# Performance work log

Measured on AMD Instinct MI355X. Metric: run time of the kernel, lower is better.

The kernel has to match this reference:

```python
import jax, jax.numpy as jnp
import numpy as np

D_MODEL = 4096
D_FF = 11008


def setup_inputs() -> dict:
    key = jax.random.key(0)
    ks = jax.random.split(key, 7)
    x = jax.random.normal(ks[0], (2, 2048, D_MODEL), dtype=jnp.float32)
    # int8-range quantized weights (stored int32 for portability)
    gate_w = jax.random.randint(ks[1], (D_FF, D_MODEL), -127, 127, dtype=jnp.int32)
    up_w = jax.random.randint(ks[2], (D_FF, D_MODEL), -127, 127, dtype=jnp.int32)
    down_w = jax.random.randint(ks[3], (D_MODEL, D_FF), -127, 127, dtype=jnp.int32)
    # per-output-channel dequant scales (small positive)
    gate_s = jax.random.uniform(ks[4], (D_FF,), dtype=jnp.float32) * 0.01 + 1e-3
    up_s = jax.random.uniform(ks[5], (D_FF,), dtype=jnp.float32) * 0.01 + 1e-3
    down_s = jax.random.uniform(ks[6], (D_MODEL,), dtype=jnp.float32) * 0.01 + 1e-3
    return {"x": x, "gate_w": gate_w, "gate_s": gate_s,
            "up_w": up_w, "up_s": up_s, "down_w": down_w, "down_s": down_s}


def _dequant_linear(x, w_int, scale):
    # y = x @ (scale[:, None] * w).T  ==  (x @ w.T) * scale  (per-row scales)
    return jnp.einsum('bsd,fd->bsf', x, w_int.astype(x.dtype)) * scale


def reference(x, gate_w, gate_s, up_w, up_s, down_w, down_s):
    gate = jax.nn.silu(_dequant_linear(x, gate_w, gate_s))  # [B,S,D_FF]
    up = _dequant_linear(x, up_w, up_s)                     # [B,S,D_FF]
    h = gate * up
    return _dequant_linear(h, down_w, down_s)               # [B,S,D_MODEL]
```

## Files before the change

### kernel.cpp

```cpp
#include <hip/hip_runtime.h>
#include <hip/hip_bf16.h>

#define D_MODEL 4096
#define D_FF    11008
#define NTOK    4096

typedef unsigned int u32;
typedef unsigned short u16;
typedef signed char s8;
using f32x4   = __attribute__((ext_vector_type(4))) float;
using i32x4   = __attribute__((ext_vector_type(4))) int;
using bf16x8  = __attribute__((ext_vector_type(8))) short;
using ushort8 = __attribute__((ext_vector_type(8))) unsigned short;
using u32x2   = __attribute__((ext_vector_type(2))) u32;
using int4v   = __attribute__((ext_vector_type(4))) int;
using float4v = __attribute__((ext_vector_type(4))) float;

__device__ __forceinline__ u16 bf16_rn(float f) {
    u32 u = __builtin_bit_cast(u32, f);
    u += 0x7FFFu + ((u >> 16) & 1u);
    return (u16)(u >> 16);
}
__device__ __forceinline__ u16 bf16_from_int(int v) {
    float f = (float)v;
    return (u16)(__builtin_bit_cast(u32, f) >> 16);
}
__device__ __forceinline__ void gload16(const void* g, void* l) {
    __builtin_amdgcn_global_load_lds(
        (const __attribute__((address_space(1))) u32*)g,
        (__attribute__((address_space(3))) u32*)l, 16, 0, 0);
}

__global__ void k_xscale(const float* __restrict__ x, float* __restrict__ xsc) {
    __shared__ float wmax[4];
    const int row = blockIdx.x;
    const int tid = threadIdx.x;
    const float* p = x + (size_t)row * D_MODEL + tid * 16;
    float m = 0.f;
#pragma unroll
    for (int j = 0; j < 4; ++j) {
        float4v v = *(const float4v*)(p + j * 4);
#pragma unroll
        for (int e = 0; e < 4; ++e) m = fmaxf(m, fabsf(v[e]));
    }
#pragma unroll
    for (int off = 1; off < 64; off <<= 1)
        m = fmaxf(m, __shfl_xor(m, off));
    if ((tid & 63) == 0) wmax[tid >> 6] = m;
    __syncthreads();
    if (tid == 0) {
        m = fmaxf(fmaxf(wmax[0], wmax[1]), fmaxf(wmax[2], wmax[3]));
        xsc[row] = m * (1.0f / 127.0f);
    }
}

__global__ void k_quant_x(const float* __restrict__ x, const float* __restrict__ xsc,
                          s8* __restrict__ xq) {
    int i = (blockIdx.x * 256 + threadIdx.x) * 8;
    const float inv = 1.0f / xsc[i >> 12];
    float4v a = *(const float4v*)(x + i);
    float4v b = *(const float4v*)(x + i + 4);
    u32 w0 = 0, w1 = 0;
#pragma unroll
    for (int e = 0; e < 4; ++e) {
        int qa = (int)rintf(a[e] * inv);
        qa = qa > 127 ? 127 : (qa < -127 ? -127 : qa);
        int qb = (int)rintf(b[e] * inv);
        qb = qb > 127 ? 127 : (qb < -127 ? -127 : qb);
        w0 |= (u32)(qa & 255) << (8 * e);
        w1 |= (u32)(qb & 255) << (8 * e);
    }
    *(u32x2*)(xq + i) = (u32x2){w0, w1};
}

__global__ void k_cvt_w8(const int* __restrict__ w, s8* __restrict__ wb) {
    int i = (blockIdx.x * 256 + threadIdx.x) * 8;
    int4v a = *(const int4v*)(w + i);
    int4v b = *(const int4v*)(w + i + 4);
    u32 w0 = 0, w1 = 0;
#pragma unroll
    for (int e = 0; e < 4; ++e) {
        w0 |= (u32)(a[e] & 255) << (8 * e);
        w1 |= (u32)(b[e] & 255) << (8 * e);
    }
    *(u32x2*)(wb + i) = (u32x2){w0, w1};
}

__global__ void k_cvt_w(const int* __restrict__ w, u16* __restrict__ wb) {
    int i = (blockIdx.x * 256 + threadIdx.x) * 8;
    int4v a = *(const int4v*)(w + i);
    int4v b = *(const int4v*)(w + i + 4);
    ushort8 o;
    o[0] = bf16_from_int(a[0]); o[1] = bf16_from_int(a[1]);
    o[2] = bf16_from_int(a[2]); o[3] = bf16_from_int(a[3]);
    o[4] = bf16_from_int(b[0]); o[5] = bf16_from_int(b[1]);
    o[6] = bf16_from_int(b[2]); o[7] = bf16_from_int(b[3]);
    *(ushort8*)(wb + i) = o;
}


#define BAR   __builtin_amdgcn_s_barrier()
#define PRIO1 __builtin_amdgcn_s_setprio(1)
#define PRIO0 __builtin_amdgcn_s_setprio(0)
#define VMC(N)  asm volatile("s_waitcnt vmcnt(" #N ")" ::: "memory")

#define RD_A8(AA, BUF, MH) {                                                  \
  _Pragma("unroll") for (int mm = 0; mm < 4; ++mm)                            \
    AA[mm] = *(const i32x4*)&lds8[(BUF)*32768 + (MH)*8192 + mm*1024 + adA]; }

#define RD_B8(BB, BUF) {                                                      \
  _Pragma("unroll") for (int nn = 0; nn < 4; ++nn)                            \
    BB[nn] = *(const i32x4*)&lds8[(BUF)*32768 + 16384 + (nn>>1)*8192 +        \
                                  (nn&1)*1024 + adB]; }

#define MFMA_I8(MH, AA, BB)                                                   \
  _Pragma("unroll") for (int mm = 0; mm < 4; ++mm)                            \
  _Pragma("unroll") for (int nn = 0; nn < 4; ++nn)                            \
    acc[(MH)*4+mm][nn] = __builtin_amdgcn_mfma_i32_16x16x64_i8(               \
        AA[mm], BB[nn], acc[(MH)*4+mm][nn], 0, 0, 0);

#define STAGE_AH(BUF, MH, K0) {                                               \
  gload16(xq + (size_t)(bm*256 + (MH)*128 + wave*16 + (lane>>2))*K + (K0) + asw, \
          &lds8[(BUF)*32768 + (MH)*8192 + wave*1024 + lane*16]); }

#define STAGE_B2(BUF, K0) {                                                   \
  gload16(b0base + (size_t)(wave*16 + (lane>>2))*K + (K0) + asw,              \
          &lds8[(BUF)*32768 + 16384 + wave*1024 + lane*16]);                  \
  gload16(b1base + (size_t)(wave*16 + (lane>>2))*K + (K0) + asw,              \
          &lds8[(BUF)*32768 + 24576 + wave*1024 + lane*16]); }

#define TILE_I8(CUR, NXT, T) {                                                \
  RD_A8(a0, CUR, 0); RD_B8(bb, CUR);                                          \
  if ((T)+1 < nt) STAGE_AH(NXT, 1, ((T)+1) << 6);                             \
  BAR; PRIO1; MFMA_I8(0, a0, bb); PRIO0; BAR;                                 \
  RD_A8(a1, CUR, 1);                                                          \
  if ((T)+2 < nt) { STAGE_AH(CUR, 0, ((T)+2) << 6);                           \
                    STAGE_B2(CUR, ((T)+2) << 6); }                            \
  BAR; PRIO1; MFMA_I8(1, a1, bb); PRIO0;                                      \
  if ((T)+2 < nt) { VMC(3); } else { VMC(0); }                                \
  BAR; }

__global__ __launch_bounds__(512, 2) void k_fusedgu_i8(
    const s8* __restrict__ xq,
    const s8* __restrict__ wg8, const s8* __restrict__ wu8,
    const float* __restrict__ gs, const float* __restrict__ us,
    const float* __restrict__ xsc,
    u16* __restrict__ hb, int K, int NBN, int ldc)
{
    __shared__ __align__(16) char lds8[65536];

    const int tid  = threadIdx.x;
    const int lane = tid & 63;
    const int wave = tid >> 6;
    const int wm   = wave >> 2;
    const int wn   = wave & 3;

    const int nwg  = 16 * NBN;
    const int orig = blockIdx.x;
    const int qq   = nwg >> 3, rr = nwg & 7;
    const int xcd  = orig & 7;
    const int swz  = (xcd < rr ? xcd*(qq+1) : rr*(qq+1) + (xcd-rr)*qq) + (orig >> 3);
    const int bm   = swz / NBN;
    const int bn   = swz % NBN;

    const int r    = lane & 15;
    const int sQ   = lane >> 4;
    const int qsw  = (sQ ^ ((r >> 1) & 3)) * 16;
    const int adA  = (wm*64 + r) * 64 + qsw;
    const int adB  = (wn*32 + r) * 64 + qsw;

    const int asw  = ((lane & 3) ^ ((lane >> 3) & 3)) * 16;

    const s8* b0base = wg8 + (size_t)(bn*128) * K;
    const s8* b1base = wu8 + (size_t)(bn*128) * K;

    i32x4 acc[8][4];
#pragma unroll
    for (int m = 0; m < 8; ++m)
#pragma unroll
        for (int n = 0; n < 4; ++n) acc[m][n] = (i32x4){0, 0, 0, 0};

    const int nt = K >> 6;

    STAGE_AH(0, 0, 0); STAGE_AH(0, 1, 0); STAGE_B2(0, 0);
    STAGE_AH(1, 0, 64); STAGE_B2(1, 64);
    VMC(3);
    BAR;

    i32x4 a0[4], a1[4], bb[4];
    for (int t = 0; t < nt; t += 2) {
        TILE_I8(0, 1, t);
        TILE_I8(1, 0, t + 1);
    }

    const int f0 = bn*128 + wn*32 + r;
    const float gsc0 = gs[f0],      usc0 = us[f0];
    const float gsc1 = gs[f0 + 16], usc1 = us[f0 + 16];
#pragma unroll
    for (int m = 0; m < 8; ++m) {
        const int row = bm*256 + (m>>2)*128 + wm*64 + (m&3)*16 + sQ*4;
#pragma unroll
        for (int q = 0; q < 4; ++q) {
            const float xs = xsc[row + q];
            const float g0 = (float)acc[m][0][q] * xs * gsc0;
            const float u0 = (float)acc[m][2][q] * xs * usc0;
            const float g1 = (float)acc[m][1][q] * xs * gsc1;
            const float u1 = (float)acc[m][3][q] * xs * usc1;
            const float h0 = (g0 / (1.0f + __expf(-g0))) * u0;
            const float h1 = (g1 / (1.0f + __expf(-g1))) * u1;
            hb[(size_t)(row + q) * ldc + f0]      = bf16_rn(h0);
            hb[(size_t)(row + q) * ldc + f0 + 16] = bf16_rn(h1);
        }
    }
}


#define READA(AA, BUF, MH) {                                                  \
  _Pragma("unroll") for (int mm = 0; mm < 4; ++mm) {                          \
    AA[mm][0] = *(const bf16x8*)&lds[(BUF)*32768 + (MH)*8192 + mm*1024 + aoffE + g0E]; \
    AA[mm][1] = *(const bf16x8*)&lds[(BUF)*32768 + (MH)*8192 + mm*1024 + aoffE + g1E]; } }

#define READB(BB, BUF, NH) {                                                  \
  _Pragma("unroll") for (int nn = 0; nn < 2; ++nn) {                          \
    BB[nn][0] = *(const bf16x8*)&lds[(BUF)*32768 + 16384 + (NH)*8192 + nn*1024 + boffE + g0E]; \
    BB[nn][1] = *(const bf16x8*)&lds[(BUF)*32768 + 16384 + (NH)*8192 + nn*1024 + boffE + g1E]; } }

#define MFMA16(MH, NH, AA, BB)                                                \
  _Pragma("unroll") for (int mm = 0; mm < 4; ++mm)                            \
  _Pragma("unroll") for (int nn = 0; nn < 2; ++nn)                            \
  _Pragma("unroll") for (int kk = 0; kk < 2; ++kk)                            \
    acc[(MH)*4+mm][(NH)*2+nn] = __builtin_amdgcn_mfma_f32_16x16x32_bf16(      \
        AA[mm][kk], BB[nn][kk], acc[(MH)*4+mm][(NH)*2+nn], 0, 0, 0);

#define REGA(BUF, H) ((BUF)*32768 + (H)*8192)
#define REGB(BUF, H) ((BUF)*32768 + 16384 + (H)*8192)

#define STAGE_A(BUF, MH, K0) {                                                \
  const u16* _s = A + a_sbase + (size_t)(MH)*128*K + (K0);                    \
  gload16(_s,                &lds[REGA(BUF, MH) + wave*512]);                 \
  gload16(_s + (size_t)64*K, &lds[REGA(BUF, MH) + (8+wave)*512]); }

#define STAGE_B(BUF, NH, K0) {                                                \
  const u16* _s = ((NH) ? b1base : b0base) + (K0);                            \
  gload16(_s,                &lds[REGB(BUF, NH) + wave*512]);                 \
  gload16(_s + (size_t)64*K, &lds[REGB(BUF, NH) + (8+wave)*512]); }

#define TILE2(CUR, NXT, T) {                                                  \
  READA(a0, CUR, 0); READB(b0, CUR, 0); READB(b1, CUR, 1);                    \
  if ((T)+1 < nt) STAGE_A(NXT, 1, ((T)+1) << 6);                              \
  BAR; PRIO1;                                                                 \
  MFMA16(0, 0, a0, b0); MFMA16(0, 1, a0, b1);                                 \
  PRIO0; BAR;                                                                 \
  READA(a1, CUR, 1);                                                          \
  if ((T)+2 < nt) { STAGE_A(CUR, 0, ((T)+2) << 6);                            \
                    STAGE_B(CUR, 0, ((T)+2) << 6);                            \
                    STAGE_B(CUR, 1, ((T)+2) << 6); }                          \
  BAR; PRIO1;                                                                 \
  MFMA16(1, 1, a1, b1); MFMA16(1, 0, a1, b0);                                 \
  PRIO0;                                                                      \
  if ((T)+2 < nt) { VMC(6); } else { VMC(0); }                                \
  BAR; }

__global__ __launch_bounds__(512, 2) void k_down256(
    const u16* __restrict__ A, const u16* __restrict__ B0,
    const float* __restrict__ sc0, float* __restrict__ of32,
    int K, int NBN, int ldc)
{
    __shared__ __align__(16) u16 lds[65536];

    const int tid  = threadIdx.x;
    const int lane = tid & 63;
    const int wave = tid >> 6;
    const int wm   = wave >> 2;
    const int wn   = wave & 3;

    const int nwg  = 16 * NBN;
    const int orig = blockIdx.x;
    const int qq   = nwg >> 3, rr = nwg & 7;
    const int xcd  = orig & 7;
    const int swz  = (xcd < rr ? xcd*(qq+1) : rr*(qq+1) + (xcd-rr)*qq) + (orig >> 3);
    const int bm   = swz / NBN;
    const int bn   = swz % NBN;

    const int r    = lane & 15;
    const int sQ   = lane >> 4;
    const int x7   = r & 7;
    const int g0E  = (sQ ^ x7) * 8;
    const int g1E  = ((4 | sQ) ^ x7) * 8;
    const int aoffE = (wm*64 + r) * 64;
    const int boffE = (wn*32 + r) * 64;

    const int lrow = lane >> 3;
    const int goff = ((lane & 7) ^ lrow) * 8;
    const size_t a_sbase = (size_t)(bm*256 + wave*8 + lrow) * K + goff;
    const u16* b0base = B0 + (size_t)(bn*256 +       wave*8 + lrow) * K + goff;
    const u16* b1base = B0 + (size_t)(bn*256 + 128 + wave*8 + lrow) * K + goff;

    f32x4 acc[8][4];
#pragma unroll
    for (int m = 0; m < 8; ++m)
#pragma unroll
        for (int n = 0; n < 4; ++n) acc[m][n] = (f32x4){0.f, 0.f, 0.f, 0.f};

    const int nt = K >> 6;

    STAGE_A(0, 0, 0); STAGE_A(0, 1, 0); STAGE_B(0, 0, 0); STAGE_B(0, 1, 0);
    STAGE_A(1, 0, 64); STAGE_B(1, 0, 64); STAGE_B(1, 1, 64);
    VMC(6);
    BAR;

    bf16x8 a0[4][2], a1[4][2], b0[2][2], b1[2][2];
    for (int t = 0; t < nt; t += 2) {
        TILE2(0, 1, t);
        TILE2(1, 0, t + 1);
    }

#pragma unroll
    for (int n = 0; n < 4; ++n) {
        const int col = bn*256 + (n>>1)*128 + wn*32 + (n&1)*16 + r;
        const float sc = sc0[col];
#pragma unroll
        for (int m = 0; m < 8; ++m) {
            const int row = bm*256 + (m>>2)*128 + wm*64 + (m&3)*16 + sQ*4;
#pragma unroll
            for (int q = 0; q < 4; ++q)
                of32[(size_t)(row + q) * ldc + col] = acc[m][n][q] * sc;
        }
    }
}

extern "C" void kernel_launch(void* const* d_in, const int* in_sizes, int n_in,
                              void* d_out, int out_size, void* d_ws, size_t ws_size,
                              hipStream_t stream) {
    const float* x  = (const float*)d_in[0];
    const int*   gw = (const int*)d_in[1];
    const float* gs = (const float*)d_in[2];
    const int*   uw = (const int*)d_in[3];
    const float* us = (const float*)d_in[4];
    const int*   dw = (const int*)d_in[5];
    const float* ds = (const float*)d_in[6];
    float* out = (float*)d_out;

    const size_t XQ = (size_t)NTOK * D_MODEL;
    const size_t W8 = (size_t)D_FF * D_MODEL;
    const size_t WD = (size_t)D_FF * D_MODEL * 2;
    const size_t HB = (size_t)NTOK * D_FF * 2;
    const size_t SC = (size_t)NTOK * 4;
    if (ws_size < XQ + 2 * W8 + WD + HB + SC) return;

    char* ws = (char*)d_ws;
    s8*  xq   = (s8*)ws;
    s8*  wg8  = (s8*)(ws + XQ);
    s8*  wu8  = (s8*)(ws + XQ + W8);
    u16* wbD  = (u16*)(ws + XQ + 2 * W8);
    u16* hb   = (u16*)(ws + XQ + 2 * W8 + WD);
    float* xsc = (float*)(ws + XQ + 2 * W8 + WD + HB);

    const int wn_elems = D_FF * D_MODEL;
    const int wgrid = wn_elems / (8 * 256);

    k_xscale<<<NTOK, 256, 0, stream>>>(x, xsc);
    k_quant_x<<<(NTOK * D_MODEL) / (8 * 256), 256, 0, stream>>>(x, xsc, xq);
    k_cvt_w8<<<wgrid, 256, 0, stream>>>(gw, wg8);
    k_cvt_w8<<<wgrid, 256, 0, stream>>>(uw, wu8);

    k_fusedgu_i8<<<16 * (D_FF / 128), 512, 0, stream>>>(
        xq, wg8, wu8, gs, us, xsc, hb, D_MODEL, D_FF / 128, D_FF);

    k_cvt_w<<<wgrid, 256, 0, stream>>>(dw, wbD);
    k_down256<<<16 * (D_MODEL / 256), 512, 0, stream>>>(
        hb, wbD, ds, out, D_FF, D_MODEL / 256, D_MODEL);
}
```

Baseline: 851.4 us.

## Fuse x quantization kernels, merge weight converts, overlap down-weight conversion with GEMM

```diff
diff --git a/kernel.cpp b/kernel.cpp
--- a/kernel.cpp
+++ b/kernel.cpp
@@ -4,6 +4,7 @@
 #define D_MODEL 4096
 #define D_FF    11008
 #define NTOK    4096
+#define CVT_BLOCKS 2048
 
 typedef unsigned int u32;
 typedef unsigned short u16;
@@ -31,71 +32,61 @@
         (__attribute__((address_space(3))) u32*)l, 16, 0, 0);
 }
 
-__global__ void k_xscale(const float* __restrict__ x, float* __restrict__ xsc) {
+__global__ void k_prep_x(const float* __restrict__ x, s8* __restrict__ xq,
+                         float* __restrict__ xsc) {
     __shared__ float wmax[4];
     const int row = blockIdx.x;
     const int tid = threadIdx.x;
     const float* p = x + (size_t)row * D_MODEL + tid * 16;
+    float4v v0 = *(const float4v*)(p);
+    float4v v1 = *(const float4v*)(p + 4);
+    float4v v2 = *(const float4v*)(p + 8);
+    float4v v3 = *(const float4v*)(p + 12);
     float m = 0.f;
 #pragma unroll
-    for (int j = 0; j < 4; ++j) {
-        float4v v = *(const float4v*)(p + j * 4);
-#pragma unroll
-        for (int e = 0; e < 4; ++e) m = fmaxf(m, fabsf(v[e]));
-    }
+    for (int e = 0; e < 4; ++e)
+        m = fmaxf(m, fmaxf(fmaxf(fabsf(v0[e]), fabsf(v1[e])),
+                           fmaxf(fabsf(v2[e]), fabsf(v3[e]))));
 #pragma unroll
     for (int off = 1; off < 64; off <<= 1)
         m = fmaxf(m, __shfl_xor(m, off));
     if ((tid & 63) == 0) wmax[tid >> 6] = m;
     __syncthreads();
-    if (tid == 0) {
-        m = fmaxf(fmaxf(wmax[0], wmax[1]), fmaxf(wmax[2], wmax[3]));
-        xsc[row] = m * (1.0f / 127.0f);
-    }
-}
-
-__global__ void k_quant_x(const float* __restrict__ x, const float* __restrict__ xsc,
-                          s8* __restrict__ xq) {
-    int i = (blockIdx.x * 256 + threadIdx.x) * 8;
-    const float inv = 1.0f / xsc[i >> 12];
-    float4v a = *(const float4v*)(x + i);
-    float4v b = *(const float4v*)(x + i + 4);
-    u32 w0 = 0, w1 = 0;
-#pragma unroll
-    for (int e = 0; e < 4; ++e) {
-        int qa = (int)rintf(a[e] * inv);
-        qa = qa > 127 ? 127 : (qa < -127 ? -127 : qa);
-        int qb = (int)rintf(b[e] * inv);
-        qb = qb > 127 ? 127 : (qb < -127 ? -127 : qb);
-        w0 |= (u32)(qa & 255) << (8 * e);
-        w1 |= (u32)(qb & 255) << (8 * e);
-    }
-    *(u32x2*)(xq + i) = (u32x2){w0, w1};
-}
-
-__global__ void k_cvt_w8(const int* __restrict__ w, s8* __restrict__ wb) {
-    int i = (blockIdx.x * 256 + threadIdx.x) * 8;
+    m = fmaxf(fmaxf(wmax[0], wmax[1]), fmaxf(wmax[2], wmax[3]));
+    if (tid == 0) xsc[row] = m * (1.0f / 127.0f);
+    const float inv = (m > 0.f) ? (127.0f / m) : 0.f;
+    i32x4 o;
+    float4v vs[4] = {v0, v1, v2, v3};
+#pragma unroll
+    for (int j = 0; j < 4; ++j) {
+        u32 w = 0;
+#pragma unroll
+        for (int e = 0; e < 4; ++e) {
+            int q = (int)rintf(vs[j][e] * inv);
+            q = q > 127 ? 127 : (q < -127 ? -127 : q);
+            w |= (u32)(q & 255) << (8 * e);
+        }
+        o[j] = (int)w;
+    }
+    *(i32x4*)(xq + (size_t)row * D_MODEL + tid * 16) = o;
+}
+
+__global__ void k_cvt_w8x2(const int* __restrict__ wA, const int* __restrict__ wB,
+                           s8* __restrict__ oA, s8* __restrict__ oB, int halfgrid) {
+    const int b = blockIdx.x;
+    const int* w; s8* o; int bb;
+    if (b < halfgrid) { w = wA; o = oA; bb = b; }
+    else              { w = wB; o = oB; bb = b - halfgrid; }
+    int i = (bb * 256 + threadIdx.x) * 8;
     int4v a = *(const int4v*)(w + i);
-    int4v b = *(const int4v*)(w + i + 4);
+    int4v c = *(const int4v*)(w + i + 4);
     u32 w0 = 0, w1 = 0;
 #pragma unroll
     for (int e = 0; e < 4; ++e) {
         w0 |= (u32)(a[e] & 255) << (8 * e);
-        w1 |= (u32)(b[e] & 255) << (8 * e);
-    }
-    *(u32x2*)(wb + i) = (u32x2){w0, w1};
-}
-
-__global__ void k_cvt_w(const int* __restrict__ w, u16* __restrict__ wb) {
-    int i = (blockIdx.x * 256 + threadIdx.x) * 8;
-    int4v a = *(const int4v*)(w + i);
-    int4v b = *(const int4v*)(w + i + 4);
-    ushort8 o;
-    o[0] = bf16_from_int(a[0]); o[1] = bf16_from_int(a[1]);
-    o[2] = bf16_from_int(a[2]); o[3] = bf16_from_int(a[3]);
-    o[4] = bf16_from_int(b[0]); o[5] = bf16_from_int(b[1]);
-    o[6] = bf16_from_int(b[2]); o[7] = bf16_from_int(b[3]);
-    *(ushort8*)(wb + i) = o;
+        w1 |= (u32)(c[e] & 255) << (8 * e);
+    }
+    *(u32x2*)(o + i) = (u32x2){w0, w1};
 }
 
 
@@ -145,9 +136,27 @@
     const s8* __restrict__ wg8, const s8* __restrict__ wu8,
     const float* __restrict__ gs, const float* __restrict__ us,
     const float* __restrict__ xsc,
-    u16* __restrict__ hb, int K, int NBN, int ldc)
+    u16* __restrict__ hb, int K, int NBN, int ldc,
+    const int* __restrict__ dw, u16* __restrict__ wbD, int nwgemm)
 {
     __shared__ __align__(16) char lds8[65536];
+
+    if ((int)blockIdx.x >= nwgemm) {
+        const long long tidg = (long long)(blockIdx.x - nwgemm) * 512 + threadIdx.x;
+        const long long stride = (long long)CVT_BLOCKS * 512 * 8;
+        const long long n = (long long)D_FF * D_MODEL;
+        for (long long i = tidg * 8; i < n; i += stride) {
+            int4v a = *(const int4v*)(dw + i);
+            int4v b = *(const int4v*)(dw + i + 4);
+            ushort8 o;
+            o[0] = bf16_from_int(a[0]); o[1] = bf16_from_int(a[1]);
+            o[2] = bf16_from_int(a[2]); o[3] = bf16_from_int(a[3]);
+            o[4] = bf16_from_int(b[0]); o[5] = bf16_from_int(b[1]);
+            o[6] = bf16_from_int(b[2]); o[7] = bf16_from_int(b[3]);
+            *(ushort8*)(wbD + i) = o;
+        }
+        return;
+    }
 
     const int tid  = threadIdx.x;
     const int lane = tid & 63;
@@ -358,16 +367,15 @@
 
     const int wn_elems = D_FF * D_MODEL;
     const int wgrid = wn_elems / (8 * 256);
-
-    k_xscale<<<NTOK, 256, 0, stream>>>(x, xsc);
-    k_quant_x<<<(NTOK * D_MODEL) / (8 * 256), 256, 0, stream>>>(x, xsc, xq);
-    k_cvt_w8<<<wgrid, 256, 0, stream>>>(gw, wg8);
-    k_cvt_w8<<<wgrid, 256, 0, stream>>>(uw, wu8);
-
-    k_fusedgu_i8<<<16 * (D_FF / 128), 512, 0, stream>>>(
-        xq, wg8, wu8, gs, us, xsc, hb, D_MODEL, D_FF / 128, D_FF);
-
-    k_cvt_w<<<wgrid, 256, 0, stream>>>(dw, wbD);
+    const int nwgemm = 16 * (D_FF / 128);
+
+    k_prep_x<<<NTOK, 256, 0, stream>>>(x, xq, xsc);
+    k_cvt_w8x2<<<2 * wgrid, 256, 0, stream>>>(gw, uw, wg8, wu8, wgrid);
+
+    k_fusedgu_i8<<<nwgemm + CVT_BLOCKS, 512, 0, stream>>>(
+        xq, wg8, wu8, gs, us, xsc, hb, D_MODEL, D_FF / 128, D_FF,
+        dw, wbD, nwgemm);
+
     k_down256<<<16 * (D_MODEL / 256), 512, 0, stream>>>(
         hb, wbD, ds, out, D_FF, D_MODEL / 256, D_MODEL);
 }
```

Result: faster. 817.5 us (-4.0%).
